# Kernel tuning notes

Hardware: AMD Instinct MI355X
Metric: run time of the kernel (lower is better)

## Reference

```python
import jax, jax.numpy as jnp
import numpy as np

N_NODES = 50000
N_EDGES = 800000


def setup_inputs() -> dict:
    key = jax.random.key(0)
    ks = jax.random.split(key, 6)
    x = jax.random.normal(ks[0], (N_NODES, 22), dtype=jnp.float32)
    # small weight scale to keep tanh in its linear-ish regime
    W0 = jax.random.normal(ks[1], (22, 220), dtype=jnp.float32) * 0.1
    W1 = jax.random.normal(ks[2], (220, 220), dtype=jnp.float32) * 0.05
    W2 = jax.random.normal(ks[3], (220, 220), dtype=jnp.float32) * 0.05
    W3 = jax.random.normal(ks[4], (220, 10), dtype=jnp.float32) * 0.05
    b0 = jnp.zeros((220,), jnp.float32)
    b1 = jnp.zeros((220,), jnp.float32)
    b2 = jnp.zeros((220,), jnp.float32)
    b3 = jnp.zeros((10,), jnp.float32)
    edge_index = jax.random.randint(ks[5], (2, N_EDGES), 0, N_NODES, dtype=jnp.int64)
    return {"x": x, "W0": W0, "b0": b0, "W1": W1, "b1": b1,
            "W2": W2, "b2": b2, "W3": W3, "b3": b3, "edge_index": edge_index}


def _graph_conv(h, W, b, src, dst, inv_sqrt_out, inv_sqrt_in, activation):
    # DGL GraphConv, norm='both':
    #   h' = D_in^{-1/2} * A^T * (D_out^{-1/2} * h) @ W + b
    h = h * inv_sqrt_out[:, None]          # [N, F_in]
    m = h[src]                             # gather: [E, F_in]
    agg = jax.ops.segment_sum(m, dst, num_segments=N_NODES)  # scatter-add: [N, F_in]
    agg = agg * inv_sqrt_in[:, None]
    out = agg @ W + b
    if activation is not None:
        out = activation(out)
    return out


def reference(x, W0, b0, W1, b1, W2, b2, W3, b3, edge_index):
    src, dst = edge_index[0], edge_index[1]
    ones = jnp.ones((edge_index.shape[1],), jnp.float32)
    deg_out = jax.ops.segment_sum(ones, src, num_segments=N_NODES)
    deg_in = jax.ops.segment_sum(ones, dst, num_segments=N_NODES)
    inv_sqrt_out = jax.lax.rsqrt(jnp.maximum(deg_out, 1.0))
    inv_sqrt_in = jax.lax.rsqrt(jnp.maximum(deg_in, 1.0))

    h = _graph_conv(x, W0, b0, src, dst, inv_sqrt_out, inv_sqrt_in, jnp.tanh)
    h = _graph_conv(h, W1, b1, src, dst, inv_sqrt_out, inv_sqrt_in, jnp.tanh)
    h = _graph_conv(h, W2, b2, src, dst, inv_sqrt_out, inv_sqrt_in, jnp.tanh)
    h = _graph_conv(h, W3, b3, src, dst, inv_sqrt_out, inv_sqrt_in, None)
    return h
```

## Files before the change

kernel.cpp:

```cpp
#include <hip/hip_runtime.h>
#include <math.h>

#define N_NODES 50000
#define N_EDGES 800000
#define NPAD 50176
#define HSTR 224

typedef __attribute__((ext_vector_type(8))) short short8;
typedef __attribute__((ext_vector_type(4))) float f32x4;
typedef __attribute__((ext_vector_type(4))) _Float16 half4;


__device__ __forceinline__ float fast_tanh(float x) {
    float e = __expf(2.0f * x);
    float r = __builtin_amdgcn_rcpf(e + 1.0f);
    return 1.0f - 2.0f * r;
}

__device__ __forceinline__ unsigned short rne_bf16(float x) {
    unsigned u = __builtin_bit_cast(unsigned, x);
    return (unsigned short)((u + 0x7FFFu + ((u >> 16) & 1u)) >> 16);
}

__device__ __forceinline__ void split_bf16(float x, unsigned short& hi, unsigned short& lo) {
    hi = rne_bf16(x);
    float hf = __builtin_bit_cast(float, (unsigned)hi << 16);
    lo = rne_bf16(x - hf);
}

__device__ __forceinline__ f32x4 mfma16(short8 a, short8 b, f32x4 c) {
    return __builtin_amdgcn_mfma_f32_16x16x32_bf16(a, b, c, 0, 0, 0);
}

__device__ __forceinline__ void wsplit_one(const float* __restrict__ W, int KIN, int LDA,
                                           unsigned short* __restrict__ WT_hi,
                                           unsigned short* __restrict__ WT_lo, int idx) {
    int n = idx / LDA;
    int k = idx - n * LDA;
    float v = (n < 220 && k < KIN) ? W[k * 220 + n] : 0.f;
    unsigned short hi, lo;
    split_bf16(v, hi, lo);
    WT_hi[idx] = hi;
    WT_lo[idx] = lo;
}


__global__ void k_hist_wsplit(const int* __restrict__ ei, int* __restrict__ deg8,
                              int* __restrict__ cnt8, int* __restrict__ rank,
                              const float* __restrict__ W0, const float* __restrict__ W1,
                              const float* __restrict__ W2,
                              unsigned short* __restrict__ wt0h, unsigned short* __restrict__ wt0l,
                              unsigned short* __restrict__ wt1h, unsigned short* __restrict__ wt1l,
                              unsigned short* __restrict__ wt2h, unsigned short* __restrict__ wt2l) {
    int bx = blockIdx.x;
    if (bx < 782) {
        int c = bx & 7;
        int* degc = deg8 + c * NPAD;
        int* cntc = cnt8 + c * NPAD;
        int base = bx * 1024 + threadIdx.x;
#pragma unroll
        for (int i = 0; i < 4; ++i) {
            int e = base + i * 256;
            if (e < N_EDGES) {
                atomicAdd(&degc[ei[e]], 1);
                int r = atomicAdd(&cntc[ei[N_EDGES + e]], 1);
                rank[e] = (r << 3) | c;
            }
        }
    } else if (bx < 810) {
        int idx = (bx - 782) * 256 + threadIdx.x;
        if (idx < 224 * 32) wsplit_one(W0, 22, 32, wt0h, wt0l, idx);
    } else if (bx < 1006) {
        int idx = (bx - 810) * 256 + threadIdx.x;
        wsplit_one(W1, 220, 224, wt1h, wt1l, idx);
    } else {
        int idx = (bx - 1006) * 256 + threadIdx.x;
        wsplit_one(W2, 220, 224, wt2h, wt2l, idx);
    }
}

__global__ void k_sum8(int* __restrict__ cnt8, const int* __restrict__ deg8,
                       int* __restrict__ ecsbuf, int* __restrict__ deg_out) {
    int d = blockIdx.x * 256 + threadIdx.x;
    if (d >= NPAD) return;
    int s = 0;
#pragma unroll
    for (int c = 0; c < 8; ++c) {
        int v = cnt8[c * NPAD + d];
        cnt8[c * NPAD + d] = s;
        s += v;
    }
    ecsbuf[1 + d] = s;
    if (d == 0) ecsbuf[0] = 0;
    int t = 0;
#pragma unroll
    for (int c = 0; c < 8; ++c) t += deg8[c * NPAD + d];
    deg_out[d] = t;
}

__global__ void k_scan1(const int* __restrict__ in, int* __restrict__ out,
                        int* __restrict__ bsum, int n) {
    __shared__ int s[256];
    int i = blockIdx.x * 256 + threadIdx.x;
    int v = (i < n) ? in[i] : 0;
    s[threadIdx.x] = v;
    __syncthreads();
    for (int off = 1; off < 256; off <<= 1) {
        int t = (threadIdx.x >= off) ? s[threadIdx.x - off] : 0;
        __syncthreads();
        s[threadIdx.x] += t;
        __syncthreads();
    }
    if (i < n) out[i] = s[threadIdx.x] - v;
    if (threadIdx.x == 255 && bsum) bsum[blockIdx.x] = s[255];
}

__global__ void k_scan_mid(int* __restrict__ a, int n) {
    __shared__ int s[256];
    __shared__ int carry;
    if (threadIdx.x == 0) carry = 0;
    for (int base = 0; base < n; base += 256) {
        int i = base + threadIdx.x;
        int v = (i < n) ? a[i] : 0;
        s[threadIdx.x] = v;
        __syncthreads();
        for (int off = 1; off < 256; off <<= 1) {
            int t = (threadIdx.x >= off) ? s[threadIdx.x - off] : 0;
            __syncthreads();
            s[threadIdx.x] += t;
            __syncthreads();
        }
        int c = carry;
        if (i < n) a[i] = s[threadIdx.x] - v + c;
        __syncthreads();
        if (threadIdx.x == 0) carry = c + s[255];
        __syncthreads();
    }
}

__global__ void k_scan3(int* __restrict__ out, const int* __restrict__ bscan, int n) {
    int i = blockIdx.x * 256 + threadIdx.x;
    if (i < n) out[i] += bscan[blockIdx.x];
}

__global__ void k_post_scan(const int* __restrict__ ei, const int* __restrict__ ecsbuf,
                            const int* __restrict__ rank, const int* __restrict__ prefix8,
                            const int* __restrict__ deg_out, const float* __restrict__ x,
                            float* __restrict__ inv_out, float* __restrict__ inv_in,
                            int* __restrict__ src_sorted, float* __restrict__ xs) {
    int bx = blockIdx.x;
    if (bx < 196) {
        int n = bx * 256 + threadIdx.x;
        if (n >= N_NODES) return;
        int di = ecsbuf[n + 2] - ecsbuf[n + 1];
        int a = deg_out[n]; if (a < 1) a = 1;
        if (di < 1) di = 1;
        inv_out[n] = 1.0f / sqrtf((float)a);
        inv_in[n]  = 1.0f / sqrtf((float)di);
    } else if (bx < 3321) {
        int e = (bx - 196) * 256 + threadIdx.x;
        if (e < N_EDGES) {
            int d = ei[N_EDGES + e];
            int rc = rank[e];
            int c = rc & 7, r = rc >> 3;
            src_sorted[ecsbuf[1 + d] + prefix8[c * NPAD + d] + r] = ei[e];
        }
    } else {
        int idx = (bx - 3321) * 256 + threadIdx.x;
        if (idx >= N_NODES * 11) return;
        int n = idx / 11;
        int f2 = idx - n * 11;
        int a = deg_out[n]; if (a < 1) a = 1;
        float sc = 1.0f / sqrtf((float)a);
        float2 v = *(const float2*)&x[n * 22 + f2 * 2];
        v.x *= sc; v.y *= sc;
        *(float2*)&xs[n * 22 + f2 * 2] = v;
    }
}


__global__ void k_agg22_split(const float* __restrict__ xs,
                              const int* __restrict__ ecsbuf, const int* __restrict__ srcs,
                              const float* __restrict__ inv_in,
                              unsigned short* __restrict__ A_hi, unsigned short* __restrict__ A_lo) {
    int idx = blockIdx.x * 256 + threadIdx.x;
    int n = idx >> 4, f2 = idx & 15;
    if (n >= N_NODES) return;
    float ax = 0.f, ay = 0.f;
    if (f2 <= 10) {
        const float2* xb = (const float2*)(xs) + f2;
        int e = ecsbuf[n + 1], end = ecsbuf[n + 2];
        for (; e + 3 < end; e += 4) {
            int s0 = srcs[e], s1 = srcs[e + 1], s2 = srcs[e + 2], s3 = srcs[e + 3];
            float2 v0 = xb[s0 * 11], v1 = xb[s1 * 11];
            float2 v2 = xb[s2 * 11], v3 = xb[s3 * 11];
            ax += (v0.x + v1.x) + (v2.x + v3.x);
            ay += (v0.y + v1.y) + (v2.y + v3.y);
        }
        for (; e < end; ++e) {
            float2 v0 = xb[srcs[e] * 11];
            ax += v0.x;
            ay += v0.y;
        }
        float si = inv_in[n];
        ax *= si; ay *= si;
    }
    ushort2 h2, l2;
    split_bf16(ax, h2.x, l2.x);
    split_bf16(ay, h2.y, l2.y);
    *(ushort2*)&A_hi[n * 32 + f2 * 2] = h2;
    *(ushort2*)&A_lo[n * 32 + f2 * 2] = l2;
}

__global__ __launch_bounds__(256) void k_agg220_split(const _Float16* __restrict__ h,
                                                      const int* __restrict__ ecsbuf,
                                                      const int* __restrict__ srcs,
                                                      const float* __restrict__ inv_in,
                                                      unsigned short* __restrict__ A_hi,
                                                      unsigned short* __restrict__ A_lo) {
    int lane = threadIdx.x & 63;
    int n = blockIdx.x * 4 + (threadIdx.x >> 6);
    if (n >= N_NODES || lane >= 56) return;
    size_t ob = (size_t)n * 224 + lane * 4;
    if (lane == 55) {
        ushort4 z = {0, 0, 0, 0};
        *(ushort4*)&A_hi[ob] = z;
        *(ushort4*)&A_lo[ob] = z;
        return;
    }
    int f4 = lane * 4;
    const _Float16* hb = h + f4;
    int e = ecsbuf[n + 1], end = ecsbuf[n + 2];
    float4 a0 = {0,0,0,0}, a1 = {0,0,0,0}, a2 = {0,0,0,0}, a3 = {0,0,0,0};
    for (; e + 7 < end; e += 8) {
        int s0 = srcs[e],     s1 = srcs[e + 1], s2 = srcs[e + 2], s3 = srcs[e + 3];
        int s4 = srcs[e + 4], s5 = srcs[e + 5], s6 = srcs[e + 6], s7 = srcs[e + 7];
        half4 v0 = *(const half4*)(hb + (size_t)s0 * HSTR);
        half4 v1 = *(const half4*)(hb + (size_t)s1 * HSTR);
        half4 v2 = *(const half4*)(hb + (size_t)s2 * HSTR);
        half4 v3 = *(const half4*)(hb + (size_t)s3 * HSTR);
        half4 v4 = *(const half4*)(hb + (size_t)s4 * HSTR);
        half4 v5 = *(const half4*)(hb + (size_t)s5 * HSTR);
        half4 v6 = *(const half4*)(hb + (size_t)s6 * HSTR);
        half4 v7 = *(const half4*)(hb + (size_t)s7 * HSTR);
        a0.x += (float)v0.x; a0.y += (float)v0.y; a0.z += (float)v0.z; a0.w += (float)v0.w;
        a1.x += (float)v1.x; a1.y += (float)v1.y; a1.z += (float)v1.z; a1.w += (float)v1.w;
        a2.x += (float)v2.x; a2.y += (float)v2.y; a2.z += (float)v2.z; a2.w += (float)v2.w;
        a3.x += (float)v3.x; a3.y += (float)v3.y; a3.z += (float)v3.z; a3.w += (float)v3.w;
        a0.x += (float)v4.x; a0.y += (float)v4.y; a0.z += (float)v4.z; a0.w += (float)v4.w;
        a1.x += (float)v5.x; a1.y += (float)v5.y; a1.z += (float)v5.z; a1.w += (float)v5.w;
        a2.x += (float)v6.x; a2.y += (float)v6.y; a2.z += (float)v6.z; a2.w += (float)v6.w;
        a3.x += (float)v7.x; a3.y += (float)v7.y; a3.z += (float)v7.z; a3.w += (float)v7.w;
    }
    for (; e + 3 < end; e += 4) {
        int s0 = srcs[e], s1 = srcs[e + 1], s2 = srcs[e + 2], s3 = srcs[e + 3];
        half4 v0 = *(const half4*)(hb + (size_t)s0 * HSTR);
        half4 v1 = *(const half4*)(hb + (size_t)s1 * HSTR);
        half4 v2 = *(const half4*)(hb + (size_t)s2 * HSTR);
        half4 v3 = *(const half4*)(hb + (size_t)s3 * HSTR);
        a0.x += (float)v0.x; a0.y += (float)v0.y; a0.z += (float)v0.z; a0.w += (float)v0.w;
        a1.x += (float)v1.x; a1.y += (float)v1.y; a1.z += (float)v1.z; a1.w += (float)v1.w;
        a2.x += (float)v2.x; a2.y += (float)v2.y; a2.z += (float)v2.z; a2.w += (float)v2.w;
        a3.x += (float)v3.x; a3.y += (float)v3.y; a3.z += (float)v3.z; a3.w += (float)v3.w;
    }
    for (; e < end; ++e) {
        half4 v = *(const half4*)(hb + (size_t)srcs[e] * HSTR);
        a0.x += (float)v.x; a0.y += (float)v.y; a0.z += (float)v.z; a0.w += (float)v.w;
    }
    float sc = inv_in[n];
    float4 t;
    t.x = ((a0.x + a1.x) + (a2.x + a3.x)) * sc;
    t.y = ((a0.y + a1.y) + (a2.y + a3.y)) * sc;
    t.z = ((a0.z + a1.z) + (a2.z + a3.z)) * sc;
    t.w = ((a0.w + a1.w) + (a2.w + a3.w)) * sc;
    ushort4 h4, l4;
    split_bf16(t.x, h4.x, l4.x);
    split_bf16(t.y, h4.y, l4.y);
    split_bf16(t.z, h4.z, l4.z);
    split_bf16(t.w, h4.w, l4.w);
    *(ushort4*)&A_hi[ob] = h4;
    *(ushort4*)&A_lo[ob] = l4;
}

__global__ void k_agg10_epi(const float* __restrict__ tmp, const int* __restrict__ ecsbuf,
                            const int* __restrict__ srcs, const float* __restrict__ inv_in,
                            const float* __restrict__ bias, float* __restrict__ out) {
    int idx = blockIdx.x * 256 + threadIdx.x;
    if (idx >= N_NODES * 5) return;
    int n = idx / 5;
    int f2 = idx - n * 5;
    const float2* tb0 = (const float2*)(tmp) + f2;
    const float2* tb1 = (const float2*)(tmp + (size_t)NPAD * 10) + f2;
    float ax = 0.f, ay = 0.f;
    int e = ecsbuf[n + 1], end = ecsbuf[n + 2];
    for (; e + 1 < end; e += 2) {
        float2 u0 = tb0[srcs[e] * 5],     w0 = tb1[srcs[e] * 5];
        float2 u1 = tb0[srcs[e + 1] * 5], w1 = tb1[srcs[e + 1] * 5];
        ax += (u0.x + w0.x) + (u1.x + w1.x);
        ay += (u0.y + w0.y) + (u1.y + w1.y);
    }
    if (e < end) {
        float2 u0 = tb0[srcs[e] * 5], w0 = tb1[srcs[e] * 5];
        ax += u0.x + w0.x;
        ay += u0.y + w0.y;
    }
    float si = inv_in[n];
    float2 o;
    o.x = ax * si + bias[f2 * 2];
    o.y = ay * si + bias[f2 * 2 + 1];
    *(float2*)&out[n * 10 + f2 * 2] = o;
}

template <int KSTEPS, int LDA, bool FUSE_W3>
__global__ __launch_bounds__(256, 4) void k_gemm_mfma(const unsigned short* __restrict__ A_hi,
                                                      const unsigned short* __restrict__ A_lo,
                                                      const unsigned short* __restrict__ WT_hi,
                                                      const unsigned short* __restrict__ WT_lo,
                                                      const float* __restrict__ bias,
                                                      const float* __restrict__ post,
                                                      _Float16* __restrict__ out,
                                                      const float* __restrict__ W3,
                                                      float* __restrict__ tmp) {
    constexpr bool SWZ = (LDA == 224);
    int tid = threadIdx.x;
    int l = tid & 63, w = tid >> 6;
    int lrow = l & 15, q = l >> 4;
    int bid = blockIdx.x;

    int ch, s = 0, v = 0, rt = 0;
    if constexpr (SWZ) {
        s = bid & 7;
        int u = bid >> 3;
        ch = u & 1;
        v = u >> 1;
    } else {
        ch = bid & 1;
        rt = (bid >> 1) * 64 + w * 16;
    }
    int cb = ch * 112;

    auto prow = [&](int i) -> int {
        if constexpr (SWZ) return 4 * s + 512 * v + 32 * (4 * w + (i >> 2)) + (i & 3);
        else return rt + i;
    };

    int arow = prow(lrow);
    const unsigned short* pah = A_hi + (size_t)arow * LDA + q * 8;
    const unsigned short* pal = A_lo + (size_t)arow * LDA + q * 8;
    const unsigned short* pbh = WT_hi + (size_t)(cb + lrow) * LDA + q * 8;
    const unsigned short* pbl = WT_lo + (size_t)(cb + lrow) * LDA + q * 8;

    f32x4 acc[7];
#pragma unroll
    for (int ct = 0; ct < 7; ++ct) acc[ct] = (f32x4){0.f, 0.f, 0.f, 0.f};

#pragma unroll
    for (int ks = 0; ks < KSTEPS; ++ks) {
        int k0 = ks * 32;
        short8 ah = *(const short8*)(const void*)(pah + k0);
        short8 al = *(const short8*)(const void*)(pal + k0);
#pragma unroll
        for (int ct = 0; ct < 7; ++ct) {
            size_t boff = (size_t)(ct * 16) * LDA + k0;
            short8 bh = *(const short8*)(const void*)(pbh + boff);
            short8 bl = *(const short8*)(const void*)(pbl + boff);
            acc[ct] = mfma16(ah, bh, acc[ct]);
            acc[ct] = mfma16(ah, bl, acc[ct]);
            acc[ct] = mfma16(al, bh, acc[ct]);
        }
    }

    float pv[4];
#pragma unroll
    for (int r = 0; r < 4; ++r) {
        int r0 = prow(q * 4 + r);
        pv[r] = (r0 < N_NODES) ? post[r0] : 0.f;
    }

    if (!FUSE_W3) {
#pragma unroll
        for (int ct = 0; ct < 7; ++ct) {
            int col = cb + ct * 16 + lrow;
            if (col >= 220) continue;
            float bv = bias[col];
#pragma unroll
            for (int r = 0; r < 4; ++r) {
                int r0 = prow(q * 4 + r);
                if (r0 < N_NODES)
                    out[(size_t)r0 * HSTR + col] = (_Float16)(pv[r] * fast_tanh(acc[ct][r] + bv));
            }
        }
    } else {
        float p[4][10];
#pragma unroll
        for (int r = 0; r < 4; ++r)
#pragma unroll
            for (int j = 0; j < 10; ++j) p[r][j] = 0.f;
#pragma unroll
        for (int ct = 0; ct < 7; ++ct) {
            int col = cb + ct * 16 + lrow;
            bool cok = col < 220;
            float bv = cok ? bias[col] : 0.f;
            float w3v[10];
            if (cok) {
                const float2* wp = (const float2*)&W3[col * 10];
#pragma unroll
                for (int j2 = 0; j2 < 5; ++j2) {
                    float2 t = wp[j2];
                    w3v[2 * j2] = t.x;
                    w3v[2 * j2 + 1] = t.y;
                }
            } else {
#pragma unroll
                for (int j = 0; j < 10; ++j) w3v[j] = 0.f;
            }
#pragma unroll
            for (int r = 0; r < 4; ++r) {
                float h2 = pv[r] * fast_tanh(acc[ct][r] + bv);
#pragma unroll
                for (int j = 0; j < 10; ++j) p[r][j] += h2 * w3v[j];
            }
        }
#pragma unroll
        for (int r = 0; r < 4; ++r)
#pragma unroll
            for (int j = 0; j < 10; ++j) {
                float vv = p[r][j];
                vv += __shfl_xor(vv, 1, 64);
                vv += __shfl_xor(vv, 2, 64);
                vv += __shfl_xor(vv, 4, 64);
                vv += __shfl_xor(vv, 8, 64);
                p[r][j] = vv;
            }
        if (lrow == 0) {
#pragma unroll
            for (int r = 0; r < 4; ++r) {
                int row = prow(q * 4 + r);
                if (row < N_NODES) {
                    float* tp = tmp + ((size_t)ch * NPAD + row) * 10;
#pragma unroll
                    for (int j2 = 0; j2 < 5; ++j2) {
                        float2 o = {p[r][2 * j2], p[r][2 * j2 + 1]};
                        *(float2*)&tp[2 * j2] = o;
                    }
                }
            }
        }
    }
}


extern "C" void kernel_launch(void* const* d_in, const int* in_sizes, int n_in,
                              void* d_out, int out_size, void* d_ws, size_t ws_size,
                              hipStream_t stream) {
    const float* x  = (const float*)d_in[0];
    const float* W0 = (const float*)d_in[1];
    const float* b0 = (const float*)d_in[2];
    const float* W1 = (const float*)d_in[3];
    const float* b1 = (const float*)d_in[4];
    const float* W2 = (const float*)d_in[5];
    const float* b2 = (const float*)d_in[6];
    const float* W3 = (const float*)d_in[7];
    const float* b3 = (const float*)d_in[8];
    const int*   ei = (const int*)d_in[9];
    float* out = (float*)d_out;

    int* ws = (int*)d_ws;
    int* ecsbuf     = ws + 0;
    int* deg_out    = ws + 50432;
    int* bsumA      = ws + 100608;
    float* inv_out  = (float*)(ws + 100864);
    float* inv_in   = (float*)(ws + 151040);
    int* src_sorted = ws + 201216;
    unsigned short* wt0h = (unsigned short*)(ws + 1001216);
    unsigned short* wt0l = (unsigned short*)(ws + 1004800);
    unsigned short* wt1h = (unsigned short*)(ws + 1008384);
    unsigned short* wt1l = (unsigned short*)(ws + 1033472);
    unsigned short* wt2h = (unsigned short*)(ws + 1058560);
    unsigned short* wt2l = (unsigned short*)(ws + 1083648);
    unsigned short* ahi  = (unsigned short*)(ws + 1108736);
    unsigned short* alo  = (unsigned short*)(ws + 6728448);
    _Float16* hbuf = (_Float16*)(ws + 12348160);
    float* tmp10 = (float*)(ws + 17948160);
    int* rank  = (int*)ahi;
    int* cnt8  = (int*)alo;
    int* deg8  = (int*)alo + 8 * NPAD;
    float* xs  = (float*)(ws + 1108736 + 3000000);

    hipMemsetAsync(cnt8, 0, (size_t)16 * NPAD * sizeof(int), stream);

    k_hist_wsplit<<<1202, 256, 0, stream>>>(ei, deg8, cnt8, rank,
                                            W0, W1, W2, wt0h, wt0l, wt1h, wt1l, wt2h, wt2l);
    k_sum8<<<196, 256, 0, stream>>>(cnt8, deg8, ecsbuf, deg_out);
    k_scan1<<<196, 256, 0, stream>>>(ecsbuf + 1, ecsbuf + 1, bsumA, NPAD);
    k_scan_mid<<<1, 256, 0, stream>>>(bsumA, 196);
    k_scan3<<<196, 256, 0, stream>>>(ecsbuf + 1, bsumA, NPAD);
    k_post_scan<<<5470, 256, 0, stream>>>(ei, ecsbuf, rank, cnt8, deg_out, x,
                                          inv_out, inv_in, src_sorted, xs);

    int gemm_grid = (NPAD / 64) * 2;
    int agg_grid  = (N_NODES + 3) / 4;

    k_agg22_split<<<(N_NODES * 16 + 255) / 256, 256, 0, stream>>>(
        xs, ecsbuf, src_sorted, inv_in, ahi, alo);
    k_gemm_mfma<1, 32, false><<<gemm_grid, 256, 0, stream>>>(
        ahi, alo, wt0h, wt0l, b0, inv_out, hbuf, nullptr, nullptr);

    k_agg220_split<<<agg_grid, 256, 0, stream>>>(hbuf, ecsbuf, src_sorted, inv_in, ahi, alo);
    k_gemm_mfma<7, 224, false><<<gemm_grid, 256, 0, stream>>>(
        ahi, alo, wt1h, wt1l, b1, inv_out, hbuf, nullptr, nullptr);

    k_agg220_split<<<agg_grid, 256, 0, stream>>>(hbuf, ecsbuf, src_sorted, inv_in, ahi, alo);
    k_gemm_mfma<7, 224, true><<<gemm_grid, 256, 0, stream>>>(
        ahi, alo, wt2h, wt2l, b2, inv_out, nullptr, W3, tmp10);

    k_agg10_epi<<<(N_NODES * 5 + 255) / 256, 256, 0, stream>>>(
        tmp10, ecsbuf, src_sorted, inv_in, b3, out);
}
```

Measured before the change: 464.2 us.

## Replace global atomic histograms with LDS-binned per-chunk histograms

```diff
diff --git a/kernel.cpp b/kernel.cpp
--- a/kernel.cpp
+++ b/kernel.cpp
@@ -5,6 +5,8 @@
 #define N_EDGES 800000
 #define NPAD 50176
 #define HSTR 224
+#define RBIN 12544
+#define NCHK 32
 
 typedef __attribute__((ext_vector_type(8))) short short8;
 typedef __attribute__((ext_vector_type(4))) float f32x4;
@@ -45,56 +47,75 @@
 }
 
 
-__global__ void k_hist_wsplit(const int* __restrict__ ei, int* __restrict__ deg8,
-                              int* __restrict__ cnt8, int* __restrict__ rank,
-                              const float* __restrict__ W0, const float* __restrict__ W1,
-                              const float* __restrict__ W2,
-                              unsigned short* __restrict__ wt0h, unsigned short* __restrict__ wt0l,
-                              unsigned short* __restrict__ wt1h, unsigned short* __restrict__ wt1l,
-                              unsigned short* __restrict__ wt2h, unsigned short* __restrict__ wt2l) {
+__global__ void k_build(const int* __restrict__ ei, int* __restrict__ deg_part,
+                        int* __restrict__ cnt_part, int* __restrict__ rank,
+                        const float* __restrict__ W0, const float* __restrict__ W1,
+                        const float* __restrict__ W2,
+                        unsigned short* __restrict__ wt0h, unsigned short* __restrict__ wt0l,
+                        unsigned short* __restrict__ wt1h, unsigned short* __restrict__ wt1l,
+                        unsigned short* __restrict__ wt2h, unsigned short* __restrict__ wt2l) {
+    __shared__ int hb[RBIN];
     int bx = blockIdx.x;
-    if (bx < 782) {
-        int c = bx & 7;
-        int* degc = deg8 + c * NPAD;
-        int* cntc = cnt8 + c * NPAD;
-        int base = bx * 1024 + threadIdx.x;
-#pragma unroll
-        for (int i = 0; i < 4; ++i) {
-            int e = base + i * 256;
-            if (e < N_EDGES) {
-                atomicAdd(&degc[ei[e]], 1);
-                int r = atomicAdd(&cntc[ei[N_EDGES + e]], 1);
-                rank[e] = (r << 3) | c;
+    if (bx < 128) {
+        int rng = bx >> 5, chk = bx & 31;
+        int lo = rng * RBIN;
+        for (int i = threadIdx.x; i < RBIN; i += 256) hb[i] = 0;
+        __syncthreads();
+        int ebeg = chk * 25000, eend = ebeg + 25000;
+        for (int e = ebeg + threadIdx.x; e < eend; e += 256) {
+            int d = ei[N_EDGES + e];
+            unsigned idx = (unsigned)(d - lo);
+            if (idx < (unsigned)RBIN) {
+                int lr = atomicAdd(&hb[idx], 1);
+                rank[e] = (lr << 5) | chk;
             }
         }
-    } else if (bx < 810) {
-        int idx = (bx - 782) * 256 + threadIdx.x;
+        __syncthreads();
+        for (int i = threadIdx.x; i < RBIN; i += 256)
+            cnt_part[chk * NPAD + lo + i] = hb[i];
+    } else if (bx < 256) {
+        int b2 = bx - 128;
+        int rng = b2 >> 5, chk = b2 & 31;
+        int lo = rng * RBIN;
+        for (int i = threadIdx.x; i < RBIN; i += 256) hb[i] = 0;
+        __syncthreads();
+        int ebeg = chk * 25000, eend = ebeg + 25000;
+        for (int e = ebeg + threadIdx.x; e < eend; e += 256) {
+            int s = ei[e];
+            unsigned idx = (unsigned)(s - lo);
+            if (idx < (unsigned)RBIN) atomicAdd(&hb[idx], 1);
+        }
+        __syncthreads();
+        for (int i = threadIdx.x; i < RBIN; i += 256)
+            deg_part[chk * NPAD + lo + i] = hb[i];
+    } else if (bx < 284) {
+        int idx = (bx - 256) * 256 + threadIdx.x;
         if (idx < 224 * 32) wsplit_one(W0, 22, 32, wt0h, wt0l, idx);
-    } else if (bx < 1006) {
-        int idx = (bx - 810) * 256 + threadIdx.x;
+    } else if (bx < 480) {
+        int idx = (bx - 284) * 256 + threadIdx.x;
         wsplit_one(W1, 220, 224, wt1h, wt1l, idx);
     } else {
-        int idx = (bx - 1006) * 256 + threadIdx.x;
+        int idx = (bx - 480) * 256 + threadIdx.x;
         wsplit_one(W2, 220, 224, wt2h, wt2l, idx);
     }
 }
 
-__global__ void k_sum8(int* __restrict__ cnt8, const int* __restrict__ deg8,
-                       int* __restrict__ ecsbuf, int* __restrict__ deg_out) {
+__global__ void k_sum32(int* __restrict__ cnt_part, const int* __restrict__ deg_part,
+                        int* __restrict__ ecsbuf, int* __restrict__ deg_out) {
     int d = blockIdx.x * 256 + threadIdx.x;
     if (d >= NPAD) return;
     int s = 0;
 #pragma unroll
-    for (int c = 0; c < 8; ++c) {
-        int v = cnt8[c * NPAD + d];
-        cnt8[c * NPAD + d] = s;
+    for (int c = 0; c < NCHK; ++c) {
+        int v = cnt_part[c * NPAD + d];
+        cnt_part[c * NPAD + d] = s;
         s += v;
     }
     ecsbuf[1 + d] = s;
     if (d == 0) ecsbuf[0] = 0;
     int t = 0;
 #pragma unroll
-    for (int c = 0; c < 8; ++c) t += deg8[c * NPAD + d];
+    for (int c = 0; c < NCHK; ++c) t += deg_part[c * NPAD + d];
     deg_out[d] = t;
 }
 
@@ -144,7 +165,7 @@
 }
 
 __global__ void k_post_scan(const int* __restrict__ ei, const int* __restrict__ ecsbuf,
-                            const int* __restrict__ rank, const int* __restrict__ prefix8,
+                            const int* __restrict__ rank, const int* __restrict__ prefix,
                             const int* __restrict__ deg_out, const float* __restrict__ x,
                             float* __restrict__ inv_out, float* __restrict__ inv_in,
                             int* __restrict__ src_sorted, float* __restrict__ xs) {
@@ -162,8 +183,8 @@
         if (e < N_EDGES) {
             int d = ei[N_EDGES + e];
             int rc = rank[e];
-            int c = rc & 7, r = rc >> 3;
-            src_sorted[ecsbuf[1 + d] + prefix8[c * NPAD + d] + r] = ei[e];
+            int c = rc & 31, r = rc >> 5;
+            src_sorted[ecsbuf[1 + d] + prefix[c * NPAD + d] + r] = ei[e];
         }
     } else {
         int idx = (bx - 3321) * 256 + threadIdx.x;
@@ -482,20 +503,18 @@
     unsigned short* alo  = (unsigned short*)(ws + 6728448);
     _Float16* hbuf = (_Float16*)(ws + 12348160);
     float* tmp10 = (float*)(ws + 17948160);
-    int* rank  = (int*)ahi;
-    int* cnt8  = (int*)alo;
-    int* deg8  = (int*)alo + 8 * NPAD;
-    float* xs  = (float*)(ws + 1108736 + 3000000);
-
-    hipMemsetAsync(cnt8, 0, (size_t)16 * NPAD * sizeof(int), stream);
-
-    k_hist_wsplit<<<1202, 256, 0, stream>>>(ei, deg8, cnt8, rank,
-                                            W0, W1, W2, wt0h, wt0l, wt1h, wt1l, wt2h, wt2l);
-    k_sum8<<<196, 256, 0, stream>>>(cnt8, deg8, ecsbuf, deg_out);
+    int* rank     = (int*)ahi;
+    int* cnt_part = (int*)alo;
+    int* deg_part = (int*)alo + NCHK * NPAD;
+    float* xs = (float*)(ws + 1108736 + 3000000);
+
+    k_build<<<676, 256, 0, stream>>>(ei, deg_part, cnt_part, rank,
+                                     W0, W1, W2, wt0h, wt0l, wt1h, wt1l, wt2h, wt2l);
+    k_sum32<<<196, 256, 0, stream>>>(cnt_part, deg_part, ecsbuf, deg_out);
     k_scan1<<<196, 256, 0, stream>>>(ecsbuf + 1, ecsbuf + 1, bsumA, NPAD);
     k_scan_mid<<<1, 256, 0, stream>>>(bsumA, 196);
     k_scan3<<<196, 256, 0, stream>>>(ecsbuf + 1, bsumA, NPAD);
-    k_post_scan<<<5470, 256, 0, stream>>>(ei, ecsbuf, rank, cnt8, deg_out, x,
+    k_post_scan<<<5470, 256, 0, stream>>>(ei, ecsbuf, rank, cnt_part, deg_out, x,
                                           inv_out, inv_in, src_sorted, xs);
 
     int gemm_grid = (NPAD / 64) * 2;
```

After: 431.3 us. 1.08x faster.
